# Optimization experiments

Hardware: AMD Instinct MI355X
Metric: run time of the kernel (lower is better)

## Reference

```python
import jax, jax.numpy as jnp
import numpy as np

LEAKY_SLOPE = 0.2

def _xavier(key, shape, gain=1.414):
    a = gain * np.sqrt(6.0 / (shape[0] + shape[1]))
    return jax.random.uniform(key, shape, minval=-a, maxval=a, dtype=jnp.float32)

C_IN, HID = 64, 128
S_SCALES = [25, 12, 5]
T_SCALES = [64, 32, 16]

def setup_inputs() -> dict:
    key = jax.random.key(0)
    ks = jax.random.split(key, 32)
    B, T, J = 256, 64, 25
    d = {}
    d["src"] = jax.random.normal(ks[0], (B, C_IN, T, J), dtype=jnp.float32)
    d["W"] = _xavier(ks[1], (C_IN, HID))
    for i in range(3):
        d[f"as_src{i}"] = _xavier(ks[2 + i], (HID, 1))
        d[f"as_dst{i}"] = _xavier(ks[5 + i], (HID, 1))
        d[f"at_src{i}"] = _xavier(ks[8 + i], (HID, 1))
        d[f"at_dst{i}"] = _xavier(ks[11 + i], (HID, 1))
    # DiffPool assignment linears: in_features -> next_scale
    d["Wsp0"] = _xavier(ks[14], (C_IN, S_SCALES[1])); d["bsp0"] = jnp.zeros((S_SCALES[1],), jnp.float32)
    d["Wsp1"] = _xavier(ks[15], (C_IN, S_SCALES[2])); d["bsp1"] = jnp.zeros((S_SCALES[2],), jnp.float32)
    d["Wtp0"] = _xavier(ks[16], (C_IN, T_SCALES[1])); d["btp0"] = jnp.zeros((T_SCALES[1],), jnp.float32)
    d["Wtp1"] = _xavier(ks[17], (C_IN, T_SCALES[2])); d["btp1"] = jnp.zeros((T_SCALES[2],), jnp.float32)
    return d


def _gat_attn(emb, a_src, a_dst):
    # emb: [N, n, H]; additive GAT scores -> [N, n, n]
    s = emb @ a_src            # [N, n, 1]
    t = emb @ a_dst            # [N, n, 1]
    return jax.nn.leaky_relu(s + jnp.swapaxes(t, -1, -2), LEAKY_SLOPE)


def _diffpool(x, attn, Wp, bp):
    # assignment S = softmax(Linear(A @ X)) : [N, n, n_next]
    S = jax.nn.softmax((attn @ x) @ Wp + bp, axis=-1)
    x_next = jnp.einsum('bnk,bnc->bkc', S, x)
    return x_next, S


def _branch(x0, W, a_srcs, a_dsts, pool_params):
    n_scales = len(a_srcs)
    attns, pools = [], []
    x_cur = x0
    for i in range(n_scales):
        emb = x_cur @ W
        attns.append(_gat_attn(emb, a_srcs[i], a_dsts[i]))
        if i < n_scales - 1:
            Wp, bp = pool_params[i]
            x_cur, S = _diffpool(x_cur, attns[i], Wp, bp)
            pools.append(S)
    fusion = attns[0]
    for i in range(1, n_scales):
        S = pools[0]
        for j in range(1, i):
            S = S @ pools[j]
        fusion = fusion + S @ attns[i] @ jnp.swapaxes(S, -1, -2)
    # dropout is identity in eval mode
    return jax.nn.softmax(fusion, axis=-1)


def reference(src, W, as_src0, as_src1, as_src2, as_dst0, as_dst1, as_dst2,
              at_src0, at_src1, at_src2, at_dst0, at_dst1, at_dst2,
              Wsp0, bsp0, Wsp1, bsp1, Wtp0, btp0, Wtp1, btp1):
    B, C_in, T, J = src.shape
    x = jnp.transpose(src, (0, 2, 3, 1))              # [B, T, J, C]
    sp_x = x.reshape(B * T, J, C_in)                   # spatial graphs
    tp_x = jnp.transpose(x, (0, 2, 1, 3)).reshape(B * J, T, C_in)  # temporal graphs

    sa = _branch(sp_x, W, [as_src0, as_src1, as_src2], [as_dst0, as_dst1, as_dst2],
                 [(Wsp0, bsp0), (Wsp1, bsp1)])
    ta = _branch(tp_x, W, [at_src0, at_src1, at_src2], [at_dst0, at_dst1, at_dst2],
                 [(Wtp0, btp0), (Wtp1, btp1)])
    return sa.reshape(B, T, J, J), ta.reshape(B, J, T, T)
```

## Files before the change

kernel.cpp:

```cpp
#include <hip/hip_runtime.h>
#include <math.h>

constexpr float LEAKY = 0.2f;

__device__ __forceinline__ float4 ldf4(const float* p){ return *reinterpret_cast<const float4*>(p); }
__device__ __forceinline__ void stf4(float* p, float4 v){ *reinterpret_cast<float4*>(p) = v; }
__device__ __forceinline__ float dot4(float4 a, float4 b){ return a.x*b.x + a.y*b.y + a.z*b.z + a.w*b.w; }
__device__ __forceinline__ float4 fma4(float s, float4 b, float4 acc){
    acc.x += s*b.x; acc.y += s*b.y; acc.z += s*b.z; acc.w += s*b.w; return acc;
}
__device__ __forceinline__ float lrelu(float f){ return f > 0.f ? f : LEAKY*f; }
__device__ __forceinline__ float4 lrelu4(float s, float4 t){
    float4 r; r.x = lrelu(s+t.x); r.y = lrelu(s+t.y); r.z = lrelu(s+t.z); r.w = lrelu(s+t.w); return r;
}
__device__ __forceinline__ float vmax4(float4 v){ return fmaxf(fmaxf(v.x,v.y), fmaxf(v.z,v.w)); }
__device__ __forceinline__ float vsum4(float4 v){ return v.x+v.y+v.z+v.w; }
__device__ __forceinline__ float4 exp4(float4 a, float mx){
    float4 r; r.x = __expf(a.x-mx); r.y = __expf(a.y-mx); r.z = __expf(a.z-mx); r.w = __expf(a.w-mx); return r;
}

__global__ void prep_kernel(const float* __restrict__ W,
    const float* a0, const float* a1, const float* a2,  const float* a3,
    const float* a4, const float* a5, const float* a6,  const float* a7,
    const float* a8, const float* a9, const float* a10, const float* a11,
    const float* __restrict__ Wsp0, const float* __restrict__ Wsp1,
    const float* __restrict__ Wtp0, const float* __restrict__ Wtp1,
    float* __restrict__ ws)
{
    int blk = blockIdx.x, t = threadIdx.x;
    if (blk < 12) {
        const float* as[12] = {a0,a1,a2,a3,a4,a5,a6,a7,a8,a9,a10,a11};
        const float* a = as[blk];
        float s = 0.f;
        #pragma unroll
        for (int h = 0; h < 128; ++h) s += W[t*128 + h] * a[h];
        ws[blk*64 + t] = s;
    } else if (blk == 12) {
        for (int i = t; i < 768; i += 64) { int k = i >> 6, c = i & 63; ws[768 + i] = Wsp0[c*12 + k]; }
    } else if (blk == 13) {
        for (int i = t; i < 320; i += 64) { int k = i >> 6, c = i & 63; ws[1536 + i] = Wsp1[c*5 + k]; }
    } else if (blk == 14) {
        for (int i = t; i < 2048; i += 64) { int k = i >> 6, c = i & 63; ws[1856 + i] = Wtp0[c*32 + k]; }
    } else {
        for (int i = t; i < 1024; i += 64) { int k = i >> 6, c = i & 63; ws[3904 + i] = Wtp1[c*16 + k]; }
    }
}

__global__ __launch_bounds__(512, 4)
void temporal_kernel(const float* __restrict__ src, const float* __restrict__ wvec_g,
                     const float* __restrict__ Wp0, const float* __restrict__ b0,
                     const float* __restrict__ Wp1, const float* __restrict__ b1,
                     float* __restrict__ out, int nwg8)
{
    constexpr int NT = 512;
    constexpr int oA1 = 0;
    constexpr int oP1 = 1152;
    constexpr int oS1 = 1792;
    constexpr int oA2 = 2432;
    constexpr int oS01 = 2752;

    __shared__ __align__(16) float xr[4352];
    __shared__ __align__(16) float A0[4352];
    __shared__ __align__(16) float PR[2304];
    __shared__ __align__(16) float S0[2304];
    __shared__ __align__(16) float sv[64], tv[64], rx[64], rs[64];
    __shared__ __align__(16) float wv[384];

    const int tid = threadIdx.x;
    const int g = (blockIdx.x & 7) * nwg8 + (blockIdx.x >> 3);
    const int b = g / 25, inner = g - b*25;

    for (int i = tid; i < 384; i += NT) wv[i] = wvec_g[i];
    for (int i = tid; i < 4096; i += NT) {
        int c = i >> 6, r = i & 63;
        xr[r*68 + c] = src[((size_t)(b*64 + c)*64 + r)*25 + inner];
    }
    __syncthreads();

    for (int i = tid; i < 128; i += NT) {
        int which = i >> 6, p = i & 63;
        const float* w = wv + which*64;
        float acc = 0.f;
        #pragma unroll
        for (int c = 0; c < 64; c += 4) acc += dot4(ldf4(&xr[p*68 + c]), ldf4(&w[c]));
        if (which) tv[p] = acc; else sv[p] = acc;
    }
    for (int i = tid; i < 512; i += NT) {
        int p = i >> 3, k4 = i & 7;
        float4 acc = {0,0,0,0};
        #pragma unroll
        for (int c = 0; c < 64; ++c) acc = fma4(xr[p*68 + c], ldf4(&Wp0[c*32 + 4*k4]), acc);
        stf4(&PR[p*36 + 4*k4], acc);
    }
    __syncthreads();

    for (int i = tid; i < 1024; i += NT) {
        int p = i >> 4, q4 = i & 15;
        stf4(&A0[p*68 + 4*q4], lrelu4(sv[p], ldf4(&tv[4*q4])));
    }
    __syncthreads();

    if (tid < 256) {
        int p = tid >> 2, k8 = tid & 3;
        float4 acc0 = ldf4(&b0[8*k8]);
        float4 acc1 = ldf4(&b0[8*k8 + 4]);
        #pragma unroll
        for (int m = 0; m < 64; ++m) {
            float a = A0[p*68 + m];
            acc0 = fma4(a, ldf4(&PR[m*36 + 8*k8]), acc0);
            acc1 = fma4(a, ldf4(&PR[m*36 + 8*k8 + 4]), acc1);
        }
        stf4(&S0[p*36 + 8*k8], acc0);
        stf4(&S0[p*36 + 8*k8 + 4], acc1);
    }
    __syncthreads();

    {
        int p = tid >> 3, l = tid & 7;
        float4 v = ldf4(&S0[p*36 + 4*l]);
        float mx = vmax4(v);
        mx = fmaxf(mx, __shfl_xor(mx,1)); mx = fmaxf(mx, __shfl_xor(mx,2)); mx = fmaxf(mx, __shfl_xor(mx,4));
        v = exp4(v, mx);
        float sm = vsum4(v);
        sm += __shfl_xor(sm,1); sm += __shfl_xor(sm,2); sm += __shfl_xor(sm,4);
        float inv = 1.f/sm;
        v.x *= inv; v.y *= inv; v.z *= inv; v.w *= inv;
        stf4(&S0[p*36 + 4*l], v);
    }
    __syncthreads();

    if (tid < 256) {
        int k = tid >> 3, c8 = tid & 7;
        float4 acc0 = {0,0,0,0}, acc1 = {0,0,0,0};
        #pragma unroll
        for (int p = 0; p < 64; ++p) {
            float s = S0[p*36 + k];
            acc0 = fma4(s, ldf4(&xr[p*68 + 8*c8]), acc0);
            acc1 = fma4(s, ldf4(&xr[p*68 + 8*c8 + 4]), acc1);
        }
        stf4(&PR[k*68 + 8*c8], acc0);
        stf4(&PR[k*68 + 8*c8 + 4], acc1);
    }
    __syncthreads();

    for (int i = tid; i < 64; i += NT) {
        int which = i >> 5, p = i & 31;
        const float* w = wv + (2 + which)*64;
        float acc = 0.f;
        #pragma unroll
        for (int c = 0; c < 64; c += 4) acc += dot4(ldf4(&PR[p*68 + c]), ldf4(&w[c]));
        if (which) tv[p] = acc; else sv[p] = acc;
    }
    for (int i = tid; i < 128; i += NT) {
        int p = i >> 2, k4 = i & 3;
        float4 acc = {0,0,0,0};
        #pragma unroll
        for (int c = 0; c < 64; ++c) acc = fma4(PR[p*68 + c], ldf4(&Wp1[c*16 + 4*k4]), acc);
        stf4(&xr[oP1 + p*20 + 4*k4], acc);
    }
    __syncthreads();

    for (int i = tid; i < 1024; i += NT) {
        int p = i >> 5, q = i & 31;
        xr[oA1 + p*36 + q] = lrelu(sv[p] + tv[q]);
    }
    __syncthreads();

    for (int i = tid; i < 128; i += NT) {
        int p = i >> 2, k4 = i & 3;
        float4 acc = ldf4(&b1[4*k4]);
        #pragma unroll
        for (int m = 0; m < 32; ++m) acc = fma4(xr[oA1 + p*36 + m], ldf4(&xr[oP1 + m*20 + 4*k4]), acc);
        stf4(&xr[oS1 + p*20 + 4*k4], acc);
    }
    __syncthreads();

    if (tid < 128) {
        int m = tid >> 2, l = tid & 3;
        float4 v = ldf4(&xr[oS1 + m*20 + 4*l]);
        float mx = vmax4(v);
        mx = fmaxf(mx, __shfl_xor(mx,1)); mx = fmaxf(mx, __shfl_xor(mx,2));
        v = exp4(v, mx);
        float sm = vsum4(v);
        sm += __shfl_xor(sm,1); sm += __shfl_xor(sm,2);
        float inv = 1.f/sm;
        v.x *= inv; v.y *= inv; v.z *= inv; v.w *= inv;
        stf4(&xr[oS1 + m*20 + 4*l], v);
    } else if (tid < 192) {
        int i = tid - 128;
        int which = i >> 5, p = i & 31;
        const float* w = wv + (4 + which)*64;
        float acc = 0.f;
        #pragma unroll
        for (int c = 0; c < 64; c += 4) acc += dot4(ldf4(&PR[p*68 + c]), ldf4(&w[c]));
        if (which) tv[p] = acc; else sv[p] = acc;
    }
    __syncthreads();

    for (int k = tid; k < 16; k += NT) {
        float a = 0.f, c2 = 0.f;
        #pragma unroll
        for (int n = 0; n < 32; ++n) { float s1 = xr[oS1 + n*20 + k]; a += s1*sv[n]; c2 += s1*tv[n]; }
        rx[k] = a; rs[k] = c2;
    }
    __syncthreads();

    for (int i = tid; i < 256; i += NT) {
        int p = i >> 4, q = i & 15;
        xr[oA2 + p*20 + q] = lrelu(rx[p] + rs[q]);
    }
    for (int i = tid; i < 512; i += NT) {
        int p = i >> 3, k4 = i & 7;
        float4 acc = {0,0,0,0};
        #pragma unroll
        for (int m = 0; m < 32; ++m) acc = fma4(S0[p*36 + m], ldf4(&xr[oA1 + m*36 + 4*k4]), acc);
        stf4(&PR[p*36 + 4*k4], acc);
    }
    __syncthreads();

    {
        int q = tid & 63, pg = tid >> 6;
        float4 s0r[8];
        #pragma unroll
        for (int j = 0; j < 8; ++j) s0r[j] = ldf4(&S0[q*36 + 4*j]);
        #pragma unroll
        for (int pi = 0; pi < 8; ++pi) {
            int p = pg*8 + pi;
            float acc = 0.f;
            #pragma unroll
            for (int j = 0; j < 8; ++j) acc += dot4(ldf4(&PR[p*36 + 4*j]), s0r[j]);
            A0[p*68 + q] += acc;
        }
    }
    for (int i = tid; i < 256; i += NT) {
        int p = i >> 2, k4 = i & 3;
        float4 acc = {0,0,0,0};
        #pragma unroll
        for (int m = 0; m < 32; ++m) acc = fma4(S0[p*36 + m], ldf4(&xr[oS1 + m*20 + 4*k4]), acc);
        stf4(&xr[oS01 + p*20 + 4*k4], acc);
    }
    __syncthreads();

    for (int i = tid; i < 256; i += NT) {
        int p = i >> 2, k4 = i & 3;
        float4 acc = {0,0,0,0};
        #pragma unroll
        for (int m = 0; m < 16; ++m) acc = fma4(xr[oS01 + p*20 + m], ldf4(&xr[oA2 + m*20 + 4*k4]), acc);
        stf4(&PR[p*20 + 4*k4], acc);
    }
    __syncthreads();

    {
        int q = tid & 63, pg = tid >> 6;
        float4 sr[4];
        #pragma unroll
        for (int j = 0; j < 4; ++j) sr[j] = ldf4(&xr[oS01 + q*20 + 4*j]);
        #pragma unroll
        for (int pi = 0; pi < 8; ++pi) {
            int p = pg*8 + pi;
            float acc = 0.f;
            #pragma unroll
            for (int j = 0; j < 4; ++j) acc += dot4(ldf4(&PR[p*20 + 4*j]), sr[j]);
            A0[p*68 + q] += acc;
        }
    }
    __syncthreads();

    {
        int p = tid >> 3, l = tid & 7;
        float4 v1 = ldf4(&A0[p*68 + 4*l]);
        float4 v2 = ldf4(&A0[p*68 + 32 + 4*l]);
        float mx = fmaxf(vmax4(v1), vmax4(v2));
        mx = fmaxf(mx, __shfl_xor(mx,1)); mx = fmaxf(mx, __shfl_xor(mx,2)); mx = fmaxf(mx, __shfl_xor(mx,4));
        float4 e1 = exp4(v1, mx), e2 = exp4(v2, mx);
        float sm = vsum4(e1) + vsum4(e2);
        sm += __shfl_xor(sm,1); sm += __shfl_xor(sm,2); sm += __shfl_xor(sm,4);
        float inv = 1.f/sm;
        e1.x*=inv; e1.y*=inv; e1.z*=inv; e1.w*=inv;
        e2.x*=inv; e2.y*=inv; e2.z*=inv; e2.w*=inv;
        size_t base = (size_t)g*4096 + (size_t)p*64;
        stf4(&out[base + 4*l], e1);
        stf4(&out[base + 32 + 4*l], e2);
    }
}

__global__ __launch_bounds__(256, 4)
void spatial_kernel(const float* __restrict__ src, const float* __restrict__ wvg,
                    const float* __restrict__ WpT0, const float* __restrict__ WpT1,
                    const float* __restrict__ b0, const float* __restrict__ b1,
                    float* __restrict__ out, int nwg8)
{
    __shared__ __align__(16) float Rx0[1700];
    __shared__ __align__(16) float RA0[700];
    __shared__ __align__(16) float RPR[816];
    __shared__ __align__(16) float RS0[500];
    __shared__ __align__(16) float sv[32], tv[32], ua[32], va[32], rxa[8], rsa[8];

    float* x0  = Rx0;
    float* A1  = Rx0;
    float* A1T = Rx0 + 240;
    float* P1T = Rx0 + 480;
    float* S1  = Rx0 + 540;
    float* S1T = Rx0 + 684;
    float* A2T = Rx0 + 744;
    float* S01 = Rx0 + 804;
    float* A0  = RA0;
    float* P0T = RPR;
    float* x1  = RPR;
    float* M1  = RPR;
    float* M2  = RPR;
    float* S0  = RS0;

    const int t = threadIdx.x;
    const int g = (blockIdx.x & 7) * nwg8 + (blockIdx.x >> 3);
    const int b = g >> 6, inner = g & 63;
    const float* srcb = src + (size_t)b*102400 + inner*25;

    for (int i = t; i < 400; i += 256) {
        int r = i % 25, c0 = (i / 25) << 2;
        float4 v;
        v.x = srcb[(c0+0)*1600 + r];
        v.y = srcb[(c0+1)*1600 + r];
        v.z = srcb[(c0+2)*1600 + r];
        v.w = srcb[(c0+3)*1600 + r];
        stf4(&x0[r*68 + c0], v);
    }
    __syncthreads();

    if (t < 50) {
        int which = t / 25, p = t - which*25;
        const float* w = wvg + which*64;
        float a = 0.f;
        #pragma unroll
        for (int c4 = 0; c4 < 16; ++c4) a += dot4(ldf4(&x0[p*68 + 4*c4]), ldf4(&w[4*c4]));
        if (which) tv[p] = a; else sv[p] = a;
    }
    for (int i = t; i < 336; i += 256) {
        int k = i / 28, m = i - k*28;
        float a = 0.f;
        if (m < 25) {
            #pragma unroll
            for (int c4 = 0; c4 < 16; ++c4) a += dot4(ldf4(&WpT0[k*64 + 4*c4]), ldf4(&x0[m*68 + 4*c4]));
        }
        P0T[k*28 + m] = a;
    }
    __syncthreads();

    for (int i = t; i < 700; i += 256) {
        int p = i / 28, q = i - p*28;
        A0[i] = (q < 25) ? lrelu(sv[p] + tv[q]) : -1e30f;
    }
    __syncthreads();

    for (int i = t; i < 300; i += 256) {
        int p = i / 12, k = i - p*12;
        float acc = b0[k];
        #pragma unroll
        for (int m4 = 0; m4 < 7; ++m4) acc += dot4(ldf4(&A0[p*28 + 4*m4]), ldf4(&P0T[k*28 + 4*m4]));
        S0[p*20 + k] = acc;
    }
    __syncthreads();

    if (t < 25) {
        float4 r[3]; float mx = -1e30f;
        #pragma unroll
        for (int u = 0; u < 3; ++u) { r[u] = ldf4(&S0[t*20 + 4*u]); mx = fmaxf(mx, vmax4(r[u])); }
        float sm = 0.f;
        #pragma unroll
        for (int u = 0; u < 3; ++u) { r[u] = exp4(r[u], mx); sm += vsum4(r[u]); }
        float inv = 1.f/sm;
        #pragma unroll
        for (int u = 0; u < 3; ++u) {
            r[u].x *= inv; r[u].y *= inv; r[u].z *= inv; r[u].w *= inv;
            stf4(&S0[t*20 + 4*u], r[u]);
        }
    }
    __syncthreads();

    if (t < 96) {
        int k = t >> 3, c0 = (t & 7) << 3;
        float4 a = {0,0,0,0}, bb = {0,0,0,0};
        #pragma unroll
        for (int p = 0; p < 25; ++p) {
            float s = S0[p*20 + k];
            a  = fma4(s, ldf4(&x0[p*68 + c0]), a);
            bb = fma4(s, ldf4(&x0[p*68 + c0 + 4]), bb);
        }
        stf4(&x1[k*68 + c0], a);
        stf4(&x1[k*68 + c0 + 4], bb);
    }
    __syncthreads();

    if (t < 48) {
        int which = t / 12, p = t - which*12;
        const float* w = wvg + (2+which)*64;
        float a = 0.f;
        #pragma unroll
        for (int c4 = 0; c4 < 16; ++c4) a += dot4(ldf4(&x1[p*68 + 4*c4]), ldf4(&w[4*c4]));
        if (which == 0) sv[p] = a; else if (which == 1) tv[p] = a;
        else if (which == 2) ua[p] = a; else va[p] = a;
    }
    for (int i = t; i < 60; i += 256) {
        int j = i / 12, k = i - j*12;
        float a = 0.f;
        #pragma unroll
        for (int c4 = 0; c4 < 16; ++c4) a += dot4(ldf4(&WpT1[j*64 + 4*c4]), ldf4(&x1[k*68 + 4*c4]));
        P1T[j*12 + k] = a;
    }
    __syncthreads();

    for (int i = t; i < 288; i += 256) {
        int mat = i / 144, rr = (i - mat*144) / 12, q = i % 12;
        if (mat == 0) A1 [rr*20 + q] = lrelu(sv[rr] + tv[q]);
        else          A1T[rr*20 + q] = lrelu(sv[q] + tv[rr]);
    }
    __syncthreads();

    for (int i = t; i < 300; i += 256) {
        int p = i / 12, k = i - p*12;
        float acc = 0.f;
        #pragma unroll
        for (int m4 = 0; m4 < 3; ++m4) acc += dot4(ldf4(&S0[p*20 + 4*m4]), ldf4(&A1T[k*20 + 4*m4]));
        M1[p*20 + k] = acc;
    }
    for (int i = t; i < 60; i += 256) {
        int m = i / 5, j = i - m*5;
        float acc = b1[j];
        #pragma unroll
        for (int k4 = 0; k4 < 3; ++k4) acc += dot4(ldf4(&A1[m*20 + 4*k4]), ldf4(&P1T[j*12 + 4*k4]));
        S1[m*12 + j] = acc;
    }
    __syncthreads();

    if (t < 12) {
        float mx = -1e30f;
        float r0 = S1[t*12+0], r1 = S1[t*12+1], r2 = S1[t*12+2], r3 = S1[t*12+3], r4 = S1[t*12+4];
        mx = fmaxf(fmaxf(fmaxf(r0,r1), fmaxf(r2,r3)), r4);
        r0 = __expf(r0-mx); r1 = __expf(r1-mx); r2 = __expf(r2-mx); r3 = __expf(r3-mx); r4 = __expf(r4-mx);
        float inv = 1.f/(r0+r1+r2+r3+r4);
        S1[t*12+0] = r0*inv; S1[t*12+1] = r1*inv; S1[t*12+2] = r2*inv; S1[t*12+3] = r3*inv; S1[t*12+4] = r4*inv;
    }
    for (int i = t; i < 625; i += 256) {
        int p = i / 25, q = i - p*25;
        float acc = A0[p*28 + q];
        #pragma unroll
        for (int m4 = 0; m4 < 3; ++m4) acc += dot4(ldf4(&M1[p*20 + 4*m4]), ldf4(&S0[q*20 + 4*m4]));
        A0[p*28 + q] = acc;
    }
    __syncthreads();

    for (int i = t; i < 60; i += 256) {
        int j = i / 12, m = i - j*12;
        S1T[j*12 + m] = S1[m*12 + j];
    }
    if (t >= 64 && t < 74) {
        int tp = t - 64, which = tp / 5, k = tp - which*5;
        float a = 0.f;
        #pragma unroll
        for (int n = 0; n < 12; ++n) a += S1[n*12 + k] * (which ? va[n] : ua[n]);
        if (which) rsa[k] = a; else rxa[k] = a;
    }
    __syncthreads();

    for (int i = t; i < 40; i += 256) {
        int q = i >> 3, p = i & 7;
        A2T[q*12 + p] = (p < 5) ? lrelu(rxa[p] + rsa[q]) : 0.f;
    }
    for (int i = t; i < 200; i += 256) {
        int p = i >> 3, c = i & 7;
        float acc = 0.f;
        if (c < 5) {
            #pragma unroll
            for (int m4 = 0; m4 < 3; ++m4) acc += dot4(ldf4(&S0[p*20 + 4*m4]), ldf4(&S1T[c*12 + 4*m4]));
        }
        S01[p*12 + c] = acc;
    }
    __syncthreads();

    for (int i = t; i < 200; i += 256) {
        int p = i >> 3, k = i & 7;
        float acc = 0.f;
        if (k < 5) {
            #pragma unroll
            for (int m4 = 0; m4 < 2; ++m4) acc += dot4(ldf4(&S01[p*12 + 4*m4]), ldf4(&A2T[k*12 + 4*m4]));
        }
        M2[p*12 + k] = acc;
    }
    __syncthreads();

    for (int i = t; i < 625; i += 256) {
        int p = i / 25, q = i - p*25;
        float acc = A0[p*28 + q];
        #pragma unroll
        for (int m4 = 0; m4 < 2; ++m4) acc += dot4(ldf4(&M2[p*12 + 4*m4]), ldf4(&S01[q*12 + 4*m4]));
        A0[p*28 + q] = acc;
    }
    __syncthreads();

    if (t < 25) {
        float4 r[7]; float mx = -1e30f;
        #pragma unroll
        for (int u = 0; u < 7; ++u) { r[u] = ldf4(&A0[t*28 + 4*u]); mx = fmaxf(mx, vmax4(r[u])); }
        float sm = 0.f;
        #pragma unroll
        for (int u = 0; u < 7; ++u) sm += vsum4(exp4(r[u], mx));
        sv[t] = mx; tv[t] = 1.f/sm;
    }
    __syncthreads();

    for (int i = t; i < 625; i += 256) {
        int p = i / 25, q = i - p*25;
        out[(size_t)g*625 + i] = __expf(A0[p*28 + q] - sv[p]) * tv[p];
    }
}

extern "C" void kernel_launch(void* const* d_in, const int* in_sizes, int n_in,
                              void* d_out, int out_size, void* d_ws, size_t ws_size,
                              hipStream_t stream) {
    const float* src = (const float*)d_in[0];
    const float* W   = (const float*)d_in[1];
    float* ws = (float*)d_ws;

    prep_kernel<<<16, 64, 0, stream>>>(W,
        (const float*)d_in[2],  (const float*)d_in[3],
        (const float*)d_in[6],  (const float*)d_in[7],
        (const float*)d_in[10], (const float*)d_in[11],
        (const float*)d_in[4],  (const float*)d_in[5],
        (const float*)d_in[8],  (const float*)d_in[9],
        (const float*)d_in[12], (const float*)d_in[13],
        (const float*)d_in[14], (const float*)d_in[16],
        (const float*)d_in[18], (const float*)d_in[20],
        ws);

    float* out = (float*)d_out;
    spatial_kernel<<<16384, 256, 0, stream>>>(
        src, ws, ws + 768, ws + 1536,
        (const float*)d_in[15], (const float*)d_in[17],
        out, 16384/8);
    temporal_kernel<<<6400, 512, 0, stream>>>(
        src, ws + 384,
        (const float*)d_in[18], (const float*)d_in[19],
        (const float*)d_in[20], (const float*)d_in[21],
        out + 10240000, 6400/8);
}
```

Before: 496.4 us.

## Fold third-scale attention into second-scale matrix before the final projection

```diff
diff --git a/kernel.cpp b/kernel.cpp
--- a/kernel.cpp
+++ b/kernel.cpp
@@ -56,8 +56,6 @@
     constexpr int oA1 = 0;
     constexpr int oP1 = 1152;
     constexpr int oS1 = 1792;
-    constexpr int oA2 = 2432;
-    constexpr int oS01 = 2752;
 
     __shared__ __align__(16) float xr[4352];
     __shared__ __align__(16) float A0[4352];
@@ -205,10 +203,27 @@
     }
     __syncthreads();
 
-    for (int i = tid; i < 256; i += NT) {
-        int p = i >> 4, q = i & 15;
-        xr[oA2 + p*20 + q] = lrelu(rx[p] + rs[q]);
-    }
+    {
+        int m = tid >> 4, k = tid & 15;
+        float rsk = rs[k];
+        float acc = 0.f;
+        #pragma unroll
+        for (int j = 0; j < 16; ++j)
+            acc += xr[oS1 + m*20 + j] * lrelu(rx[j] + rsk);
+        xr[oP1 + m*20 + k] = acc;
+    }
+    __syncthreads();
+
+    for (int i = tid; i < 1024; i += NT) {
+        int m = i >> 5, n = i & 31;
+        float acc = xr[oA1 + m*36 + n];
+        #pragma unroll
+        for (int j4 = 0; j4 < 4; ++j4)
+            acc += dot4(ldf4(&xr[oP1 + m*20 + 4*j4]), ldf4(&xr[oS1 + n*20 + 4*j4]));
+        xr[oA1 + m*36 + n] = acc;
+    }
+    __syncthreads();
+
     for (int i = tid; i < 512; i += NT) {
         int p = i >> 3, k4 = i & 7;
         float4 acc = {0,0,0,0};
@@ -229,38 +244,6 @@
             float acc = 0.f;
             #pragma unroll
             for (int j = 0; j < 8; ++j) acc += dot4(ldf4(&PR[p*36 + 4*j]), s0r[j]);
-            A0[p*68 + q] += acc;
-        }
-    }
-    for (int i = tid; i < 256; i += NT) {
-        int p = i >> 2, k4 = i & 3;
-        float4 acc = {0,0,0,0};
-        #pragma unroll
-        for (int m = 0; m < 32; ++m) acc = fma4(S0[p*36 + m], ldf4(&xr[oS1 + m*20 + 4*k4]), acc);
-        stf4(&xr[oS01 + p*20 + 4*k4], acc);
-    }
-    __syncthreads();
-
-    for (int i = tid; i < 256; i += NT) {
-        int p = i >> 2, k4 = i & 3;
-        float4 acc = {0,0,0,0};
-        #pragma unroll
-        for (int m = 0; m < 16; ++m) acc = fma4(xr[oS01 + p*20 + m], ldf4(&xr[oA2 + m*20 + 4*k4]), acc);
-        stf4(&PR[p*20 + 4*k4], acc);
-    }
-    __syncthreads();
-
-    {
-        int q = tid & 63, pg = tid >> 6;
-        float4 sr[4];
-        #pragma unroll
-        for (int j = 0; j < 4; ++j) sr[j] = ldf4(&xr[oS01 + q*20 + 4*j]);
-        #pragma unroll
-        for (int pi = 0; pi < 8; ++pi) {
-            int p = pg*8 + pi;
-            float acc = 0.f;
-            #pragma unroll
-            for (int j = 0; j < 4; ++j) acc += dot4(ldf4(&PR[p*20 + 4*j]), sr[j]);
             A0[p*68 + q] += acc;
         }
     }
```

After: 482.8 us. -2.7%, faster.
